# Kernel optimization log

Measured on AMD Instinct MI355X. Metric: run time of the kernel, lower is better.

## Reference

```python
import jax, jax.numpy as jnp
import numpy as np

B, W, C_BLK, N_EMBD, N_HEADS = 512, 128, 24, 32, 2


def setup_inputs() -> dict:
    key = jax.random.key(0)
    k1, k2, k3, k4 = jax.random.split(key, 4)
    x = jax.random.normal(k1, (B, W, C_BLK, N_EMBD), dtype=jnp.float32)
    x_end_idx = jax.random.randint(k2, (B, W), 0, C_BLK, dtype=jnp.int32)
    # nn.Linear(n_embd, 3*n_embd, bias=False): store transposed so y = x @ w
    w_attn = jax.random.normal(k3, (N_EMBD, 3 * N_EMBD), dtype=jnp.float32) * (1.0 / np.sqrt(N_EMBD))
    w_proj = jax.random.normal(k4, (N_EMBD, N_EMBD), dtype=jnp.float32) * (1.0 / np.sqrt(N_EMBD))
    return {"x": x, "x_end_idx": x_end_idx, "w_attn": w_attn, "w_proj": w_proj}


def reference(x, x_end_idx, w_attn, w_proj):
    # x: [B, W, c, C]; causal self-attention over the char axis c, per (batch, word).
    Bd, Wd, c, C = x.shape
    H = N_HEADS
    D = C // H
    qkv = x @ w_attn                               # [B, W, c, 3C]
    q, k, v = jnp.split(qkv, 3, axis=-1)
    # [B, W, H, c, D]
    q = q.reshape(Bd, Wd, c, H, D).transpose(0, 1, 3, 2, 4)
    k = k.reshape(Bd, Wd, c, H, D).transpose(0, 1, 3, 2, 4)
    v = v.reshape(Bd, Wd, c, H, D).transpose(0, 1, 3, 2, 4)
    scale = 1.0 / jnp.sqrt(jnp.asarray(D, dtype=x.dtype))
    scores = jnp.einsum('bwhqd,bwhkd->bwhqk', q, k) * scale   # [B, W, H, c, c]
    causal = jnp.tril(jnp.ones((c, c), dtype=bool))
    scores = jnp.where(causal, scores, jnp.asarray(-jnp.inf, dtype=scores.dtype))
    att = jax.nn.softmax(scores, axis=-1)
    out = jnp.einsum('bwhqk,bwhkd->bwhqd', att, v)            # [B, W, H, c, D]
    out = out.transpose(0, 1, 3, 2, 4).reshape(Bd, Wd, c, C)
    out = out @ w_proj                                        # c_proj (dropout in eval mode = identity)
    out = x + out                                             # residual
    # Vectorized last-token gather: pick out[b, w, x_end_idx[b, w], :]
    idx = x_end_idx[:, :, None, None].astype(jnp.int32)       # [B, W, 1, 1]
    samples = jnp.take_along_axis(out, jnp.broadcast_to(idx, (Bd, Wd, 1, C)), axis=2)
    return samples.squeeze(2)                                 # [B, W, C]
```

## Files before the change

kernel.cpp:

```cpp
#include <hip/hip_runtime.h>


#define CB     24
#define CC     32
#define NH     2
#define DD     16
#define THREEC 96

__global__ __launch_bounds__(64, 4) void char_attn_kernel(
    const float* __restrict__ x,
    const int*   __restrict__ xend,
    const float* __restrict__ w_attn,
    const float* __restrict__ w_proj,
    float*       __restrict__ out)
{
    __shared__ float xs[CB][CC];
    __shared__ float ks[CB][CC + 1];
    __shared__ float qs[CC];
    __shared__ float ps[NH][32];
    __shared__ float os[CC];

    const int bid  = blockIdx.x;
    const int lane = threadIdx.x;
    const float* xb = x + (size_t)bid * (CB * CC);
    const int qidx = xend[bid];
    const int L    = qidx + 1;

    {
        const float4* xb4 = (const float4*)xb;
        float4* xs4 = (float4*)&xs[0][0];
        const int n4 = L * (CC / 4);
        for (int t = lane; t < n4; t += 64) xs4[t] = xb4[t];
    }

    float wkv[CC];
    #pragma unroll
    for (int c = 0; c < CC; ++c) wkv[c] = w_attn[c * THREEC + 32 + lane];

    __syncthreads();

    float vreg[CB];
    #pragma unroll
    for (int j = 0; j < CB; ++j) {
        if (j < L) {
            const float4* row = (const float4*)&xs[j][0];
            float acc = 0.f;
            #pragma unroll
            for (int c4 = 0; c4 < CC / 4; ++c4) {
                float4 r = row[c4];
                acc += r.x * wkv[c4 * 4 + 0];
                acc += r.y * wkv[c4 * 4 + 1];
                acc += r.z * wkv[c4 * 4 + 2];
                acc += r.w * wkv[c4 * 4 + 3];
            }
            if (lane < CC) ks[j][lane] = acc;
            else           vreg[j]    = acc;
        }
    }

    if (lane < CC) {
        const float4* row = (const float4*)&xs[qidx][0];
        float acc = 0.f;
        #pragma unroll
        for (int c4 = 0; c4 < CC / 4; ++c4) {
            float4 r = row[c4];
            acc += r.x * w_attn[(c4 * 4 + 0) * THREEC + lane];
            acc += r.y * w_attn[(c4 * 4 + 1) * THREEC + lane];
            acc += r.z * w_attn[(c4 * 4 + 2) * THREEC + lane];
            acc += r.w * w_attn[(c4 * 4 + 3) * THREEC + lane];
        }
        qs[lane] = acc;
    }

    __syncthreads();

    {
        const int h = lane >> 5;
        const int j = lane & 31;
        float s = -INFINITY;
        if (j <= qidx) {
            float acc = 0.f;
            #pragma unroll
            for (int d = 0; d < DD; ++d)
                acc += qs[h * DD + d] * ks[j][h * DD + d];
            s = acc * 0.25f;
        }
        float m = s;
        #pragma unroll
        for (int off = 16; off >= 1; off >>= 1)
            m = fmaxf(m, __shfl_xor(m, off));
        float e = (j <= qidx) ? __expf(s - m) : 0.f;
        float sum = e;
        #pragma unroll
        for (int off = 16; off >= 1; off >>= 1)
            sum += __shfl_xor(sum, off);
        ps[h][j] = e / sum;
    }

    __syncthreads();

    if (lane >= CC) {
        const int dp = lane - CC;
        const int h  = dp >> 4;
        float acc = 0.f;
        #pragma unroll
        for (int j = 0; j < CB; ++j)
            if (j < L) acc += ps[h][j] * vreg[j];
        os[dp] = acc;
    }

    __syncthreads();

    if (lane >= CC) {
        const int i = lane - CC;
        float acc = xs[qidx][i];
        #pragma unroll
        for (int c = 0; c < CC; ++c)
            acc += os[c] * w_proj[c * CC + i];
        out[(size_t)bid * CC + i] = acc;
    }
}

extern "C" void kernel_launch(void* const* d_in, const int* in_sizes, int n_in,
                              void* d_out, int out_size, void* d_ws, size_t ws_size,
                              hipStream_t stream) {
    const float* x      = (const float*)d_in[0];
    const int*   xend   = (const int*)d_in[1];
    const float* w_attn = (const float*)d_in[2];
    const float* w_proj = (const float*)d_in[3];
    float* out = (float*)d_out;

    const int nbw = 512 * 128;
    char_attn_kernel<<<dim3(nbw), dim3(64), 0, stream>>>(x, xend, w_attn, w_proj, out);
}
```

Baseline: 333.4 us.

## Make kernel persistent with one wave per word and shared weight tiles

Replaces one 64-thread block per (batch, word) with a persistent grid of 256-thread blocks, where each wave loops over words in a grid-stride fashion. The q and proj weights are staged once per block into LDS, and block barriers are replaced by per-wave s_waitcnt fences. x rows are read straight from global memory instead of being staged in LDS, and the q and proj dot products are split across both half-waves and combined with a shuffle. The aim is to cut launch and block-scheduling overhead, repeated weight loads and barrier cost. The trade-off is that correctness now depends on wave-local LDS ordering through waitcnt alone.

```diff
diff --git a/kernel.cpp b/kernel.cpp
--- a/kernel.cpp
+++ b/kernel.cpp
@@ -1,123 +1,179 @@
 #include <hip/hip_runtime.h>
 
 
-#define CB     24
-#define CC     32
-#define NH     2
-#define DD     16
-#define THREEC 96
+#define CB      24
+#define CC      32
+#define DD      16
+#define THREEC  96
+#define NBW     (512 * 128)
+#define NBLOCKS 1536
+#define WPB     4
+#define TOTAL_WAVES (NBLOCKS * WPB)
 
-__global__ __launch_bounds__(64, 4) void char_attn_kernel(
+struct __align__(16) WaveSmem {
+    float ks[CB][36];
+    float qs[CC];
+    float ps[2][CC];
+    float os[CC];
+};
+
+__device__ __forceinline__ void wave_fence() {
+    __asm__ volatile("s_waitcnt lgkmcnt(0)" ::: "memory");
+}
+
+__global__ __launch_bounds__(256, 6) void char_attn_kernel(
     const float* __restrict__ x,
     const int*   __restrict__ xend,
     const float* __restrict__ w_attn,
     const float* __restrict__ w_proj,
     float*       __restrict__ out)
 {
-    __shared__ float xs[CB][CC];
-    __shared__ float ks[CB][CC + 1];
-    __shared__ float qs[CC];
-    __shared__ float ps[NH][32];
-    __shared__ float os[CC];
+    __shared__ float wqs[CC][CC];
+    __shared__ float wps[CC][CC];
+    __shared__ WaveSmem sm[WPB];
 
-    const int bid  = blockIdx.x;
-    const int lane = threadIdx.x;
-    const float* xb = x + (size_t)bid * (CB * CC);
-    const int qidx = xend[bid];
-    const int L    = qidx + 1;
+    const int tid  = threadIdx.x;
+    const int lane = tid & 63;
+    const int wave = __builtin_amdgcn_readfirstlane(tid >> 6);
+    WaveSmem& S = sm[wave];
 
-    {
-        const float4* xb4 = (const float4*)xb;
-        float4* xs4 = (float4*)&xs[0][0];
-        const int n4 = L * (CC / 4);
-        for (int t = lane; t < n4; t += 64) xs4[t] = xb4[t];
+    for (int t = tid; t < CC * CC; t += 256) {
+        const int c = t >> 5, i = t & 31;
+        wqs[c][i] = w_attn[c * THREEC + i];
+        wps[c][i] = w_proj[t];
     }
+    __syncthreads();
 
     float wkv[CC];
     #pragma unroll
-    for (int c = 0; c < CC; ++c) wkv[c] = w_attn[c * THREEC + 32 + lane];
+    for (int c = 0; c < CC; ++c) wkv[c] = w_attn[c * THREEC + CC + lane];
 
-    __syncthreads();
+    const int i32  = lane & 31;
+    const int half = lane >> 5;
 
     float vreg[CB];
     #pragma unroll
-    for (int j = 0; j < CB; ++j) {
-        if (j < L) {
-            const float4* row = (const float4*)&xs[j][0];
-            float acc = 0.f;
+    for (int j = 0; j < CB; ++j) vreg[j] = 0.f;
+
+    const int wgid = blockIdx.x * WPB + wave;
+
+    for (int bid = wgid; bid < NBW; bid += TOTAL_WAVES) {
+        const int qidx = xend[bid];
+        const int L    = qidx + 1;
+        const float* xb = x + (size_t)bid * (CB * CC);
+
+        #pragma unroll
+        for (int j = 0; j < CB; ++j) {
+            if (j < L) {
+                const float4* xr = (const float4*)(xb + j * CC);
+                float a0 = 0.f, a1 = 0.f, a2 = 0.f, a3 = 0.f;
+                #pragma unroll
+                for (int c4 = 0; c4 < 8; c4 += 4) {
+                    float4 r0 = xr[c4 + 0], r1 = xr[c4 + 1];
+                    float4 r2 = xr[c4 + 2], r3 = xr[c4 + 3];
+                    const int c = c4 * 4;
+                    a0 = fmaf(r0.x, wkv[c + 0], a0);  a1 = fmaf(r0.y, wkv[c + 1], a1);
+                    a2 = fmaf(r0.z, wkv[c + 2], a2);  a3 = fmaf(r0.w, wkv[c + 3], a3);
+                    a0 = fmaf(r1.x, wkv[c + 4], a0);  a1 = fmaf(r1.y, wkv[c + 5], a1);
+                    a2 = fmaf(r1.z, wkv[c + 6], a2);  a3 = fmaf(r1.w, wkv[c + 7], a3);
+                    a0 = fmaf(r2.x, wkv[c + 8], a0);  a1 = fmaf(r2.y, wkv[c + 9], a1);
+                    a2 = fmaf(r2.z, wkv[c + 10], a2); a3 = fmaf(r2.w, wkv[c + 11], a3);
+                    a0 = fmaf(r3.x, wkv[c + 12], a0); a1 = fmaf(r3.y, wkv[c + 13], a1);
+                    a2 = fmaf(r3.z, wkv[c + 14], a2); a3 = fmaf(r3.w, wkv[c + 15], a3);
+                }
+                const float acc = (a0 + a1) + (a2 + a3);
+                if (lane < CC) S.ks[j][lane] = acc;
+                else           vreg[j]      = acc;
+            }
+        }
+
+        {
+            const float4* xq = (const float4*)(xb + qidx * CC);
+            float a0 = 0.f, a1 = 0.f;
             #pragma unroll
-            for (int c4 = 0; c4 < CC / 4; ++c4) {
-                float4 r = row[c4];
-                acc += r.x * wkv[c4 * 4 + 0];
-                acc += r.y * wkv[c4 * 4 + 1];
-                acc += r.z * wkv[c4 * 4 + 2];
-                acc += r.w * wkv[c4 * 4 + 3];
+            for (int c4 = 0; c4 < 4; ++c4) {
+                float4 r = xq[half * 4 + c4];
+                const int c = half * 16 + c4 * 4;
+                a0 = fmaf(r.x, wqs[c + 0][i32], a0);
+                a1 = fmaf(r.y, wqs[c + 1][i32], a1);
+                a0 = fmaf(r.z, wqs[c + 2][i32], a0);
+                a1 = fmaf(r.w, wqs[c + 3][i32], a1);
             }
-            if (lane < CC) ks[j][lane] = acc;
-            else           vreg[j]    = acc;
+            float t = a0 + a1;
+            t += __shfl_xor(t, 32);
+            if (lane < CC) S.qs[i32] = t * 0.25f;
         }
-    }
 
-    if (lane < CC) {
-        const float4* row = (const float4*)&xs[qidx][0];
-        float acc = 0.f;
-        #pragma unroll
-        for (int c4 = 0; c4 < CC / 4; ++c4) {
-            float4 r = row[c4];
-            acc += r.x * w_attn[(c4 * 4 + 0) * THREEC + lane];
-            acc += r.y * w_attn[(c4 * 4 + 1) * THREEC + lane];
-            acc += r.z * w_attn[(c4 * 4 + 2) * THREEC + lane];
-            acc += r.w * w_attn[(c4 * 4 + 3) * THREEC + lane];
+        wave_fence();
+
+        {
+            const int j2 = i32;
+            float s = -INFINITY;
+            if (j2 <= qidx) {
+                const float4* kr = (const float4*)&S.ks[j2][half * DD];
+                const float4* qr = (const float4*)&S.qs[half * DD];
+                float a0 = 0.f, a1 = 0.f;
+                #pragma unroll
+                for (int t = 0; t < 4; ++t) {
+                    float4 kk = kr[t], qq = qr[t];
+                    a0 = fmaf(kk.x, qq.x, a0);
+                    a1 = fmaf(kk.y, qq.y, a1);
+                    a0 = fmaf(kk.z, qq.z, a0);
+                    a1 = fmaf(kk.w, qq.w, a1);
+                }
+                s = a0 + a1;
+            }
+            float m = s;
+            #pragma unroll
+            for (int off = 16; off >= 1; off >>= 1)
+                m = fmaxf(m, __shfl_xor(m, off));
+            const float e = (j2 <= qidx) ? __expf(s - m) : 0.f;
+            float sum = e;
+            #pragma unroll
+            for (int off = 16; off >= 1; off >>= 1)
+                sum += __shfl_xor(sum, off);
+            S.ps[half][j2] = e / sum;
         }
-        qs[lane] = acc;
-    }
 
-    __syncthreads();
+        wave_fence();
 
-    {
-        const int h = lane >> 5;
-        const int j = lane & 31;
-        float s = -INFINITY;
-        if (j <= qidx) {
-            float acc = 0.f;
+        if (lane >= CC) {
+            const int dp = lane - CC;
+            const int h  = dp >> 4;
+            const float4* pr = (const float4*)S.ps[h];
+            float a0 = 0.f, a1 = 0.f;
             #pragma unroll
-            for (int d = 0; d < DD; ++d)
-                acc += qs[h * DD + d] * ks[j][h * DD + d];
-            s = acc * 0.25f;
+            for (int t = 0; t < 6; ++t) {
+                float4 p4 = pr[t];
+                a0 = fmaf(p4.x, vreg[4 * t + 0], a0);
+                a1 = fmaf(p4.y, vreg[4 * t + 1], a1);
+                a0 = fmaf(p4.z, vreg[4 * t + 2], a0);
+                a1 = fmaf(p4.w, vreg[4 * t + 3], a1);
+            }
+            S.os[dp] = a0 + a1;
         }
-        float m = s;
-        #pragma unroll
-        for (int off = 16; off >= 1; off >>= 1)
-            m = fmaxf(m, __shfl_xor(m, off));
-        float e = (j <= qidx) ? __expf(s - m) : 0.f;
-        float sum = e;
-        #pragma unroll
-        for (int off = 16; off >= 1; off >>= 1)
-            sum += __shfl_xor(sum, off);
-        ps[h][j] = e / sum;
-    }
 
-    __syncthreads();
+        wave_fence();
 
-    if (lane >= CC) {
-        const int dp = lane - CC;
-        const int h  = dp >> 4;
-        float acc = 0.f;
-        #pragma unroll
-        for (int j = 0; j < CB; ++j)
-            if (j < L) acc += ps[h][j] * vreg[j];
-        os[dp] = acc;
-    }
+        {
+            const float4* o4 = (const float4*)S.os;
+            float a0 = 0.f, a1 = 0.f;
+            #pragma unroll
+            for (int c4 = 0; c4 < 4; ++c4) {
+                float4 o = o4[half * 4 + c4];
+                const int c = half * 16 + c4 * 4;
+                a0 = fmaf(o.x, wps[c + 0][i32], a0);
+                a1 = fmaf(o.y, wps[c + 1][i32], a1);
+                a0 = fmaf(o.z, wps[c + 2][i32], a0);
+                a1 = fmaf(o.w, wps[c + 3][i32], a1);
+            }
+            float t = a0 + a1;
+            t += __shfl_xor(t, 32);
+            if (lane < CC)
+                out[(size_t)bid * CC + lane] = t + xb[qidx * CC + lane];
+        }
 
-    __syncthreads();
-
-    if (lane >= CC) {
-        const int i = lane - CC;
-        float acc = xs[qidx][i];
-        #pragma unroll
-        for (int c = 0; c < CC; ++c)
-            acc += os[c] * w_proj[c * CC + i];
-        out[(size_t)bid * CC + i] = acc;
+        wave_fence();
     }
 }
 
@@ -130,6 +186,5 @@
     const float* w_proj = (const float*)d_in[3];
     float* out = (float*)d_out;
 
-    const int nbw = 512 * 128;
-    char_attn_kernel<<<dim3(nbw), dim3(64), 0, stream>>>(x, xend, w_attn, w_proj, out);
+    char_attn_kernel<<<dim3(NBLOCKS), dim3(256), 0, stream>>>(x, xend, w_attn, w_proj, out);
 }
```

Result: slower. 502.9 us (+50.8%).
